# Kernel tuning notes

Hardware: AMD Instinct MI355X
Metric: run time of the kernel (lower is better)

## Reference

```python
import jax, jax.numpy as jnp
import numpy as np

B, T, C = 2, 2048, 2048
N_HEAD, N_GROUP = 32, 8
HEAD_DIM = C // N_HEAD           # 64
HIG = N_HEAD // N_GROUP          # heads per group = 4


def setup_inputs() -> dict:
    key = jax.random.key(0)
    ks = jax.random.split(key, 8)
    s = 1.0 / np.sqrt(C)
    return {
        "q": jax.random.normal(ks[0], (B, T, C), jnp.float32),
        "k": jax.random.normal(ks[1], (B, T, C), jnp.float32),
        "v": jax.random.normal(ks[2], (B, T, C), jnp.float32),
        "Wq": jax.random.normal(ks[3], (C, C), jnp.float32) * s,
        "Wk": jax.random.normal(ks[4], (N_GROUP * HEAD_DIM, C), jnp.float32) * s,
        "Wv": jax.random.normal(ks[5], (N_GROUP * HEAD_DIM, C), jnp.float32) * s,
        "Wp": jax.random.normal(ks[6], (C, C), jnp.float32) * s,
        "bp": jax.random.normal(ks[7], (C,), jnp.float32) * s,
    }


def reference(q, k, v, Wq, Wk, Wv, Wp, bp):
    # Q projection -> (B, HIG, G, T, D); head h = i*G + g (row-major split of n_head)
    qp = (q @ Wq.T).reshape(B, T, N_HEAD, HEAD_DIM)
    qp = qp.transpose(0, 2, 1, 3).reshape(B, HIG, N_GROUP, T, HEAD_DIM)
    # K/V projections -> (B, G, T, D), shared across heads within a group
    kp = (k @ Wk.T).reshape(B, T, N_GROUP, HEAD_DIM).transpose(0, 2, 1, 3)
    vp = (v @ Wv.T).reshape(B, T, N_GROUP, HEAD_DIM).transpose(0, 2, 1, 3)
    scale = 1.0 / jnp.sqrt(jnp.asarray(HEAD_DIM, qp.dtype))
    scores = jnp.einsum('bigtd,bgsd->bigts', qp, kp) * scale  # (B,HIG,G,T,T)
    attn = jax.nn.softmax(scores, axis=-1)
    out = jnp.einsum('bigts,bgsd->bigtd', attn, vp)           # (B,HIG,G,T,D)
    out = out.reshape(B, N_HEAD, T, HEAD_DIM).transpose(0, 2, 1, 3).reshape(B, T, C)
    return out @ Wp.T + bp  # dropout is identity in eval mode
```

## Files before the change

kernel.cpp:

```cpp
#include <hip/hip_runtime.h>

#define DEVI __device__ __forceinline__

typedef __bf16 bf16_t;
typedef __bf16 bf16x8 __attribute__((ext_vector_type(8)));
typedef __bf16 bf16x4v __attribute__((ext_vector_type(4)));
typedef float f32x4 __attribute__((ext_vector_type(4)));

#define CSL 0.18033688011112042f

DEVI void async16(void* lds, const void* g) {
  __builtin_amdgcn_global_load_lds(
      (const __attribute__((address_space(1))) unsigned int*)g,
      (__attribute__((address_space(3))) unsigned int*)lds, 16, 0, 0);
}

__global__ __launch_bounds__(256) void cvt3(const float* __restrict__ a,
                                            const float* __restrict__ b,
                                            const float* __restrict__ c,
                                            bf16_t* __restrict__ da,
                                            bf16_t* __restrict__ db,
                                            bf16_t* __restrict__ dc, int n) {
  const float* s = (blockIdx.y == 0) ? a : (blockIdx.y == 1) ? b : c;
  bf16_t* d = (blockIdx.y == 0) ? da : (blockIdx.y == 1) ? db : dc;
  const int i = (blockIdx.x * 256 + threadIdx.x) * 4;
  if (i < n) {
    const float4 f = *(const float4*)(s + i);
    bf16x4v o;
    o.x = (bf16_t)f.x; o.y = (bf16_t)f.y; o.z = (bf16_t)f.z; o.w = (bf16_t)f.w;
    *(bf16x4v*)(d + i) = o;
  }
}
__global__ __launch_bounds__(256) void cvt2(const float* __restrict__ a,
                                            const float* __restrict__ b,
                                            bf16_t* __restrict__ da,
                                            bf16_t* __restrict__ db, int n) {
  const float* s = (blockIdx.y == 0) ? a : b;
  bf16_t* d = (blockIdx.y == 0) ? da : db;
  const int i = (blockIdx.x * 256 + threadIdx.x) * 4;
  if (i < n) {
    const float4 f = *(const float4*)(s + i);
    bf16x4v o;
    o.x = (bf16_t)f.x; o.y = (bf16_t)f.y; o.z = (bf16_t)f.z; o.w = (bf16_t)f.w;
    *(bf16x4v*)(d + i) = o;
  }
}

template<int MODE>
DEVI void gemm_core(const bf16_t* __restrict__ A, const bf16_t* __restrict__ W,
                    const float* __restrict__ bias, void* __restrict__ outv,
                    int N, int K, int bx, int by)
{
  __shared__ __align__(16) bf16_t Al[128 * 32];
  __shared__ __align__(16) bf16_t Bl[128 * 32];
  const int t = threadIdx.x;
  const int w = t >> 6, lane = t & 63;
  const int l15 = lane & 15, quad = lane >> 4;
  const int wm = (w >> 1) * 64, wn = (w & 1) * 64;
  const int m0 = by * 128, n0 = bx * 128;
  const int srow = t >> 2;
  const int skc = (t & 3) * 8;

  f32x4 acc[4][4] = {};

  for (int kk = 0; kk < K; kk += 32) {
    __syncthreads();
#pragma unroll
    for (int i = 0; i < 2; ++i) {
      async16(Al + i * 2048 + w * 512,
              A + (size_t)(m0 + i * 64 + srow) * K + kk + skc);
      async16(Bl + i * 2048 + w * 512,
              W + (size_t)(n0 + i * 64 + srow) * K + kk + skc);
    }
    __syncthreads();
    bf16x8 af[4], bfr[4];
#pragma unroll
    for (int x = 0; x < 4; ++x) {
      af[x]  = *(const bf16x8*)&Al[(wm + x * 16 + l15) * 32 + quad * 8];
      bfr[x] = *(const bf16x8*)&Bl[(wn + x * 16 + l15) * 32 + quad * 8];
    }
#pragma unroll
    for (int mt = 0; mt < 4; ++mt)
#pragma unroll
      for (int nt = 0; nt < 4; ++nt)
        acc[mt][nt] = __builtin_amdgcn_mfma_f32_16x16x32_bf16(af[mt], bfr[nt], acc[mt][nt], 0, 0, 0);
  }

#pragma unroll
  for (int mt = 0; mt < 4; ++mt) {
#pragma unroll
    for (int nt = 0; nt < 4; ++nt) {
      const int n = n0 + wn + nt * 16 + l15;
#pragma unroll
      for (int r = 0; r < 4; ++r) {
        const int m = m0 + wm + mt * 16 + quad * 4 + r;
        const float v = acc[mt][nt][r];
        if (MODE == 0) {
          ((bf16_t*)outv)[(size_t)m * N + n] = (bf16_t)v;
        } else if (MODE == 1) {
          ((float*)outv)[(size_t)m * N + n] = v + bias[n];
        } else if (MODE == 2) {
          ((bf16_t*)outv)[(size_t)(m >> 11) * (512 * 2048) + (size_t)n * 2048 + (m & 2047)] = (bf16_t)v;
        } else {
          ((bf16_t*)outv)[(size_t)m * N + n] = (bf16_t)(v * CSL);
        }
      }
    }
  }
}

__global__ __launch_bounds__(256) void gemm_scaled(const bf16_t* __restrict__ A,
                                                   const bf16_t* __restrict__ W,
                                                   bf16_t* __restrict__ out, int N, int K) {
  gemm_core<3>(A, W, nullptr, out, N, K, blockIdx.x, blockIdx.y);
}
__global__ __launch_bounds__(256) void gemm_bias_f32(const bf16_t* __restrict__ A,
                                                     const bf16_t* __restrict__ W,
                                                     const float* __restrict__ bias,
                                                     float* __restrict__ out, int N, int K) {
  gemm_core<1>(A, W, bias, out, N, K, blockIdx.x, blockIdx.y);
}
__global__ __launch_bounds__(256) void gemm_kv(const bf16_t* __restrict__ kin,
                                               const bf16_t* __restrict__ Wk,
                                               bf16_t* __restrict__ kp,
                                               const bf16_t* __restrict__ vin,
                                               const bf16_t* __restrict__ Wv,
                                               bf16_t* __restrict__ vt) {
  if (blockIdx.z == 0) gemm_core<0>(kin, Wk, nullptr, kp, 512, 2048, blockIdx.x, blockIdx.y);
  else                 gemm_core<2>(vin, Wv, nullptr, vt, 512, 2048, blockIdx.x, blockIdx.y);
}

__global__ __launch_bounds__(256) void attn_kernel(
    const bf16_t* __restrict__ Qp, const bf16_t* __restrict__ Kp,
    const bf16_t* __restrict__ Vt, bf16_t* __restrict__ O)
{
  __shared__ __align__(16) bf16_t Kl[64 * 72];
  __shared__ __align__(16) bf16_t Vl[64 * 72];
  __shared__ __align__(16) bf16_t Pl[4 * 32 * 72];

  const int t = threadIdx.x;
  const int w = t >> 6, lane = t & 63;
  const int l15 = lane & 15, quad = lane >> 4;
  const int h = blockIdx.y, b = blockIdx.z, g = h & 7;
  const int t0 = blockIdx.x * 128 + w * 32;

  const size_t qbase = (size_t)b * (2048u * 2048u) + (size_t)h * 64;
  const size_t kbase = (size_t)b * (2048u * 512u) + (size_t)g * 64;
  const size_t vbase = (size_t)b * (512u * 2048u) + (size_t)(g * 64) * 2048u;

  bf16x8 qf[2][2];
#pragma unroll
  for (int nt = 0; nt < 2; ++nt)
#pragma unroll
    for (int kc = 0; kc < 2; ++kc)
      qf[nt][kc] = *(const bf16x8*)&Qp[qbase + (size_t)(t0 + nt * 16 + l15) * 2048 + kc * 32 + quad * 8];

  f32x4 oacc[2][4] = {};
  float rs[2] = {0.f, 0.f};

  const int srow = t >> 3;
  const int sc8 = (t & 7) * 8;

  for (int it = 0; it < 32; ++it) {
    const int s0 = it * 64;
    __syncthreads();
    bf16x8 kreg[2], vreg[2];
#pragma unroll
    for (int i = 0; i < 2; ++i) {
      const int row = i * 32 + srow;
      kreg[i] = *(const bf16x8*)&Kp[kbase + (size_t)(s0 + row) * 512 + sc8];
      vreg[i] = *(const bf16x8*)&Vt[vbase + (size_t)row * 2048 + s0 + sc8];
    }
#pragma unroll
    for (int i = 0; i < 2; ++i) {
      const int row = i * 32 + srow;
      *(bf16x8*)&Kl[row * 72 + sc8] = kreg[i];
      *(bf16x8*)&Vl[row * 72 + sc8] = vreg[i];
    }
    __syncthreads();

    f32x4 sacc[4][2] = {};
#pragma unroll
    for (int kc = 0; kc < 2; ++kc) {
#pragma unroll
      for (int kt = 0; kt < 4; ++kt) {
        bf16x8 kf = *(const bf16x8*)&Kl[(kt * 16 + l15) * 72 + kc * 32 + quad * 8];
#pragma unroll
        for (int nt = 0; nt < 2; ++nt)
          sacc[kt][nt] = __builtin_amdgcn_mfma_f32_16x16x32_bf16(kf, qf[nt][kc], sacc[kt][nt], 0, 0, 0);
      }
    }

#pragma unroll
    for (int nt = 0; nt < 2; ++nt) {
#pragma unroll
      for (int kt = 0; kt < 4; ++kt) {
        const float p0 = exp2f(sacc[kt][nt][0]);
        const float p1 = exp2f(sacc[kt][nt][1]);
        const float p2 = exp2f(sacc[kt][nt][2]);
        const float p3 = exp2f(sacc[kt][nt][3]);
        rs[nt] += (p0 + p1) + (p2 + p3);
        bf16x4v o;
        o.x = (bf16_t)p0; o.y = (bf16_t)p1; o.z = (bf16_t)p2; o.w = (bf16_t)p3;
        *(bf16x4v*)&Pl[w * 2304 + (nt * 16 + l15) * 72 + kt * 16 + quad * 4] = o;
      }
    }

#pragma unroll
    for (int kc = 0; kc < 2; ++kc) {
      bf16x8 pf[2];
#pragma unroll
      for (int mt = 0; mt < 2; ++mt)
        pf[mt] = *(const bf16x8*)&Pl[w * 2304 + (mt * 16 + l15) * 72 + kc * 32 + quad * 8];
#pragma unroll
      for (int db = 0; db < 4; ++db) {
        bf16x8 vf = *(const bf16x8*)&Vl[(db * 16 + l15) * 72 + kc * 32 + quad * 8];
#pragma unroll
        for (int mt = 0; mt < 2; ++mt)
          oacc[mt][db] = __builtin_amdgcn_mfma_f32_16x16x32_bf16(pf[mt], vf, oacc[mt][db], 0, 0, 0);
      }
    }
  }

  float linv[2][4];
#pragma unroll
  for (int nt = 0; nt < 2; ++nt) {
    float rl = rs[nt];
    rl += __shfl_xor(rl, 16);
    rl += __shfl_xor(rl, 32);
#pragma unroll
    for (int r = 0; r < 4; ++r)
      linv[nt][r] = 1.0f / __shfl(rl, quad * 4 + r);
  }

#pragma unroll
  for (int mt = 0; mt < 2; ++mt)
#pragma unroll
    for (int db = 0; db < 4; ++db)
#pragma unroll
      for (int r = 0; r < 4; ++r) {
        const int tt = t0 + mt * 16 + quad * 4 + r;
        const int d = db * 16 + l15;
        O[((size_t)(b * 2048 + tt) * 32 + h) * 64 + d] = (bf16_t)(oacc[mt][db][r] * linv[mt][r]);
      }
}

extern "C" void kernel_launch(void* const* d_in, const int* in_sizes, int n_in,
                              void* d_out, int out_size, void* d_ws, size_t ws_size,
                              hipStream_t stream) {
  const float* q  = (const float*)d_in[0];
  const float* k  = (const float*)d_in[1];
  const float* v  = (const float*)d_in[2];
  const float* Wq = (const float*)d_in[3];
  const float* Wk = (const float*)d_in[4];
  const float* Wv = (const float*)d_in[5];
  const float* Wp = (const float*)d_in[6];
  const float* bp = (const float*)d_in[7];
  float* out = (float*)d_out;

  bf16_t* ws = (bf16_t*)d_ws;
  bf16_t* qb  = ws;
  bf16_t* kb  = ws +  8388608;
  bf16_t* vb  = ws + 16777216;
  bf16_t* Wqb = ws + 25165824;
  bf16_t* Wkb = ws + 29360128;
  bf16_t* Wvb = ws + 30408704;
  bf16_t* Wpb = ws + 31457280;
  bf16_t* Qp  = ws + 35651584;
  bf16_t* Kp  = ws + 44040192;
  bf16_t* Vt  = ws + 46137344;
  bf16_t* Ob  = qb;

  cvt3<<<dim3(8192, 3), 256, 0, stream>>>(q, k, v, qb, kb, vb, 8388608);
  cvt2<<<dim3(4096, 2), 256, 0, stream>>>(Wq, Wp, Wqb, Wpb, 4194304);
  cvt2<<<dim3(1024, 2), 256, 0, stream>>>(Wk, Wv, Wkb, Wvb, 1048576);

  gemm_scaled<<<dim3(16, 32), 256, 0, stream>>>(qb, Wqb, Qp, 2048, 2048);
  gemm_kv<<<dim3(4, 32, 2), 256, 0, stream>>>(kb, Wkb, Kp, vb, Wvb, Vt);
  attn_kernel<<<dim3(16, 32, 2), 256, 0, stream>>>(Qp, Kp, Vt, Ob);
  gemm_bias_f32<<<dim3(16, 32), 256, 0, stream>>>(Ob, Wpb, bp, out, 2048, 2048);
}
```

Baseline: 436.1 us.

## Load K/V MFMA fragments directly from global, compute row sums via MFMA

The attention kernel no longer stages K and V tiles through shared memory with two barriers per iteration. Each wave instead loads its MFMA operand fragments straight from global memory, relying on L2/cache reuse across waves. The softmax row sum is now computed by an extra MFMA of P against a ones vector, which replaces the scalar accumulation and shuffle reduction. Exp and reciprocal use hardware intrinsics, and the bf16 packing uses a perm-based rounding. Dropping LDS staging removes barrier stalls, but each wave now issues redundant global loads, and the packing rounds ties differently from the previous conversion.

```diff
diff --git a/kernel.cpp b/kernel.cpp
--- a/kernel.cpp
+++ b/kernel.cpp
@@ -130,12 +130,16 @@
   else                 gemm_core<2>(vin, Wv, nullptr, vt, 512, 2048, blockIdx.x, blockIdx.y);
 }
 
+DEVI unsigned pack2(float hi, float lo) {
+  return __builtin_amdgcn_perm(__builtin_bit_cast(unsigned, hi) + 0x8000u,
+                               __builtin_bit_cast(unsigned, lo) + 0x8000u,
+                               0x07060302u);
+}
+
 __global__ __launch_bounds__(256) void attn_kernel(
     const bf16_t* __restrict__ Qp, const bf16_t* __restrict__ Kp,
     const bf16_t* __restrict__ Vt, bf16_t* __restrict__ O)
 {
-  __shared__ __align__(16) bf16_t Kl[64 * 72];
-  __shared__ __align__(16) bf16_t Vl[64 * 72];
   __shared__ __align__(16) bf16_t Pl[4 * 32 * 72];
 
   const int t = threadIdx.x;
@@ -155,54 +159,61 @@
     for (int kc = 0; kc < 2; ++kc)
       qf[nt][kc] = *(const bf16x8*)&Qp[qbase + (size_t)(t0 + nt * 16 + l15) * 2048 + kc * 32 + quad * 8];
 
+  const bf16_t* pK[4];
+  const bf16_t* pV[4];
+#pragma unroll
+  for (int kt = 0; kt < 4; ++kt)
+    pK[kt] = Kp + kbase + (size_t)(kt * 16 + l15) * 512 + quad * 8;
+#pragma unroll
+  for (int db = 0; db < 4; ++db)
+    pV[db] = Vt + vbase + (size_t)(db * 16 + l15) * 2048 + quad * 8;
+
   f32x4 oacc[2][4] = {};
-  float rs[2] = {0.f, 0.f};
-
-  const int srow = t >> 3;
-  const int sc8 = (t & 7) * 8;
+  f32x4 lacc[2] = {};
+  bf16x8 onesf;
+#pragma unroll
+  for (int j = 0; j < 8; ++j) onesf[j] = (bf16_t)1.0f;
 
   for (int it = 0; it < 32; ++it) {
-    const int s0 = it * 64;
-    __syncthreads();
-    bf16x8 kreg[2], vreg[2];
-#pragma unroll
-    for (int i = 0; i < 2; ++i) {
-      const int row = i * 32 + srow;
-      kreg[i] = *(const bf16x8*)&Kp[kbase + (size_t)(s0 + row) * 512 + sc8];
-      vreg[i] = *(const bf16x8*)&Vt[vbase + (size_t)row * 2048 + s0 + sc8];
-    }
-#pragma unroll
-    for (int i = 0; i < 2; ++i) {
-      const int row = i * 32 + srow;
-      *(bf16x8*)&Kl[row * 72 + sc8] = kreg[i];
-      *(bf16x8*)&Vl[row * 72 + sc8] = vreg[i];
-    }
-    __syncthreads();
+    bf16x8 kf[4][2];
+#pragma unroll
+    for (int kt = 0; kt < 4; ++kt)
+#pragma unroll
+      for (int kc = 0; kc < 2; ++kc)
+        kf[kt][kc] = *(const bf16x8*)(pK[kt] + kc * 32);
+#pragma unroll
+    for (int kt = 0; kt < 4; ++kt) pK[kt] += 64 * 512;
 
     f32x4 sacc[4][2] = {};
 #pragma unroll
-    for (int kc = 0; kc < 2; ++kc) {
+    for (int kc = 0; kc < 2; ++kc)
+#pragma unroll
+      for (int kt = 0; kt < 4; ++kt)
+#pragma unroll
+        for (int nt = 0; nt < 2; ++nt)
+          sacc[kt][nt] = __builtin_amdgcn_mfma_f32_16x16x32_bf16(kf[kt][kc], qf[nt][kc], sacc[kt][nt], 0, 0, 0);
+
+    bf16x8 vf[4][2];
+#pragma unroll
+    for (int db = 0; db < 4; ++db)
+#pragma unroll
+      for (int kc = 0; kc < 2; ++kc)
+        vf[db][kc] = *(const bf16x8*)(pV[db] + kc * 32);
+#pragma unroll
+    for (int db = 0; db < 4; ++db) pV[db] += 64;
+
+#pragma unroll
+    for (int nt = 0; nt < 2; ++nt) {
 #pragma unroll
       for (int kt = 0; kt < 4; ++kt) {
-        bf16x8 kf = *(const bf16x8*)&Kl[(kt * 16 + l15) * 72 + kc * 32 + quad * 8];
-#pragma unroll
-        for (int nt = 0; nt < 2; ++nt)
-          sacc[kt][nt] = __builtin_amdgcn_mfma_f32_16x16x32_bf16(kf, qf[nt][kc], sacc[kt][nt], 0, 0, 0);
-      }
-    }
-
-#pragma unroll
-    for (int nt = 0; nt < 2; ++nt) {
-#pragma unroll
-      for (int kt = 0; kt < 4; ++kt) {
-        const float p0 = exp2f(sacc[kt][nt][0]);
-        const float p1 = exp2f(sacc[kt][nt][1]);
-        const float p2 = exp2f(sacc[kt][nt][2]);
-        const float p3 = exp2f(sacc[kt][nt][3]);
-        rs[nt] += (p0 + p1) + (p2 + p3);
-        bf16x4v o;
-        o.x = (bf16_t)p0; o.y = (bf16_t)p1; o.z = (bf16_t)p2; o.w = (bf16_t)p3;
-        *(bf16x4v*)&Pl[w * 2304 + (nt * 16 + l15) * 72 + kt * 16 + quad * 4] = o;
+        const float p0 = __builtin_amdgcn_exp2f(sacc[kt][nt][0]);
+        const float p1 = __builtin_amdgcn_exp2f(sacc[kt][nt][1]);
+        const float p2 = __builtin_amdgcn_exp2f(sacc[kt][nt][2]);
+        const float p3 = __builtin_amdgcn_exp2f(sacc[kt][nt][3]);
+        uint2 u;
+        u.x = pack2(p1, p0);
+        u.y = pack2(p3, p2);
+        *(uint2*)&Pl[w * 2304 + (nt * 16 + l15) * 72 + kt * 16 + quad * 4] = u;
       }
     }
 
@@ -213,36 +224,31 @@
       for (int mt = 0; mt < 2; ++mt)
         pf[mt] = *(const bf16x8*)&Pl[w * 2304 + (mt * 16 + l15) * 72 + kc * 32 + quad * 8];
 #pragma unroll
+      for (int mt = 0; mt < 2; ++mt)
+        lacc[mt] = __builtin_amdgcn_mfma_f32_16x16x32_bf16(pf[mt], onesf, lacc[mt], 0, 0, 0);
+#pragma unroll
       for (int db = 0; db < 4; ++db) {
-        bf16x8 vf = *(const bf16x8*)&Vl[(db * 16 + l15) * 72 + kc * 32 + quad * 8];
 #pragma unroll
         for (int mt = 0; mt < 2; ++mt)
-          oacc[mt][db] = __builtin_amdgcn_mfma_f32_16x16x32_bf16(pf[mt], vf, oacc[mt][db], 0, 0, 0);
-      }
-    }
-  }
-
-  float linv[2][4];
-#pragma unroll
-  for (int nt = 0; nt < 2; ++nt) {
-    float rl = rs[nt];
-    rl += __shfl_xor(rl, 16);
-    rl += __shfl_xor(rl, 32);
-#pragma unroll
-    for (int r = 0; r < 4; ++r)
-      linv[nt][r] = 1.0f / __shfl(rl, quad * 4 + r);
-  }
-
-#pragma unroll
-  for (int mt = 0; mt < 2; ++mt)
+          oacc[mt][db] = __builtin_amdgcn_mfma_f32_16x16x32_bf16(pf[mt], vf[db][kc], oacc[mt][db], 0, 0, 0);
+      }
+    }
+  }
+
+#pragma unroll
+  for (int mt = 0; mt < 2; ++mt) {
+    float linv[4];
+#pragma unroll
+    for (int r = 0; r < 4; ++r) linv[r] = __builtin_amdgcn_rcpf(lacc[mt][r]);
 #pragma unroll
     for (int db = 0; db < 4; ++db)
 #pragma unroll
       for (int r = 0; r < 4; ++r) {
         const int tt = t0 + mt * 16 + quad * 4 + r;
         const int d = db * 16 + l15;
-        O[((size_t)(b * 2048 + tt) * 32 + h) * 64 + d] = (bf16_t)(oacc[mt][db][r] * linv[mt][r]);
-      }
+        O[((size_t)(b * 2048 + tt) * 32 + h) * 64 + d] = (bf16_t)(oacc[mt][db][r] * linv[r]);
+      }
+  }
 }
 
 extern "C" void kernel_launch(void* const* d_in, const int* in_sizes, int n_in,
```

After: 604.5 us. +38.6%, slower.
